# Kernel tuning notes

Hardware: AMD Instinct MI355X
Metric: run time of the kernel (lower is better)

## Reference

```python
import jax, jax.numpy as jnp
import numpy as np


def _conv(x, w, pad):
    # NCHW conv, stride 1
    return jax.lax.conv_general_dilated(
        x, w, window_strides=(1, 1), padding=pad,
        dimension_numbers=('NCHW', 'OIHW', 'NCHW'))


def setup_inputs() -> dict:
    key = jax.random.key(0)
    ks = jax.random.split(key, 8)
    N, Cin, H, W = 8, 512, 64, 64
    Cout, scale = 128, 2
    sd = 0.02
    return {
        'x':     jax.random.normal(ks[0], (N, Cin, H, W), jnp.float32),
        'w_du':  jax.random.normal(ks[1], (Cout, Cin, 3, 1), jnp.float32) * sd,
        'b_du':  jnp.zeros((Cout,), jnp.float32),
        'w_lr':  jax.random.normal(ks[2], (Cout, Cin, 1, 3), jnp.float32) * sd,
        'b_lr':  jnp.zeros((Cout,), jnp.float32),
        'w_1x1': jax.random.normal(ks[3], (Cout, Cin, 1, 1), jnp.float32) * sd,
        'w_ch':  jax.random.normal(ks[4], (Cout, 3 * Cout, 1, 1), jnp.float32) * sd,
        'w_w':   jax.random.normal(ks[5], (Cout * scale, Cout, 1, 1), jnp.float32) * sd,
        'w_H':   jax.random.normal(ks[6], (Cout * scale, Cout, 1, 1), jnp.float32) * sd,
        'scale': scale,
    }


def _conv_du(x, w, b):
    # convDU3, stride=1: the (3,1) conv is applied to each 1-tall row slice with
    # padding (1,0); rows are folded into the batch dim (vectorized, same math).
    N, C, H, W = x.shape
    rows = x.transpose(0, 2, 1, 3).reshape(N * H, C, 1, W)
    y = _conv(rows, w, ((1, 1), (0, 0))) + b[None, :, None, None]
    y = jax.nn.relu(y)                       # (N*H, Cout, 1, W)
    Co = y.shape[1]
    return y.reshape(N, H, Co, W).transpose(0, 2, 1, 3)


def _conv_lr(x, w, b):
    # convLR3, stride=1: (1,3) conv per 1-wide column slice; columns -> batch.
    N, C, H, W = x.shape
    cols = x.transpose(0, 3, 1, 2).reshape(N * W, C, H, 1)
    y = _conv(cols, w, ((0, 0), (1, 1))) + b[None, :, None, None]
    y = jax.nn.relu(y)                       # (N*W, Cout, H, 1)
    Co = y.shape[1]
    return y.reshape(N, W, Co, H).transpose(0, 2, 3, 1)


def reference(x, w_du, b_du, w_lr, b_lr, w_1x1, w_ch, w_w, w_H, scale):
    xdu = _conv_du(x, w_du, b_du)
    xlr = _conv_lr(x, w_lr, b_lr)
    x1 = _conv(x, w_1x1, ((0, 0), (0, 0)))
    x = jnp.concatenate((x1, xlr, xdu), axis=1)
    x = _conv(x, w_ch, ((0, 0), (0, 0)))
    x = _conv(x, w_w, ((0, 0), (0, 0)))      # (N, Cout*scale, H, W)
    N, C, H, W = x.shape
    # height pixel-shuffle: channels -> height
    xp = x.transpose(0, 3, 2, 1).reshape(N, W, H * scale, C // scale)
    xp = xp.transpose(0, 3, 2, 1)            # (N, Cout, H*scale, W)
    xh = _conv(xp, w_H, ((0, 0), (0, 0)))    # (N, Cout*scale, H*scale, W)
    # width pixel-shuffle: channels -> width
    xh = xh.transpose(0, 2, 3, 1).reshape(N, H * scale, W * scale, C // scale)
    return xh.transpose(0, 3, 1, 2)          # (N, Cout, H*scale, W*scale)
```

## Files before the change

### kernel.cpp

```cpp
#include <hip/hip_runtime.h>
#include <hip/hip_bf16.h>
#include <stdint.h>
#include <stddef.h>


typedef __attribute__((ext_vector_type(8))) __bf16 bf16x8;
typedef __attribute__((ext_vector_type(4))) float  f32x4;
typedef __attribute__((ext_vector_type(2))) float  f32x2;
typedef __attribute__((ext_vector_type(4))) unsigned int u32x4;
typedef __attribute__((ext_vector_type(2))) unsigned int u32x2;

#define BAR() asm volatile("s_waitcnt lgkmcnt(0)\n\ts_barrier" ::: "memory")



__global__ __launch_bounds__(256) void prep_k(
    const float* __restrict__ w_ch, const float* __restrict__ w_1x1,
    const float* __restrict__ w_lr, const float* __restrict__ w_du,
    const float* __restrict__ w_H,  const float* __restrict__ w_w,
    __bf16* __restrict__ Wf, __bf16* __restrict__ W2f)
{
  __shared__ float wh[2][128];
  __shared__ float Mrow[2][128];
  int bid = blockIdx.x;
  if (bid < 768) {
    int gid = bid * 256 + threadIdx.x;
    int r = gid >> 9, c = gid & 511;
    float v;
    if (r < 128) {
      const float* a_ = w_ch + r * 384;
      const float* b_ = w_1x1 + c;
      float s0 = 0.f, s1 = 0.f, s2 = 0.f, s3 = 0.f;
      #pragma unroll
      for (int j = 0; j < 128; j += 4) {
        s0 += a_[j + 0] * b_[(size_t)(j + 0) * 512];
        s1 += a_[j + 1] * b_[(size_t)(j + 1) * 512];
        s2 += a_[j + 2] * b_[(size_t)(j + 2) * 512];
        s3 += a_[j + 3] * b_[(size_t)(j + 3) * 512];
      }
      v = (s0 + s1) + (s2 + s3);
    } else if (r < 256) {
      v = w_lr[(r - 128) * 1536 + c * 3 + 1];
    } else {
      v = w_du[(r - 256) * 1536 + c * 3 + 1];
    }
    int gks = c >> 5, lsub = (c >> 3) & 3, jj = c & 7;
    int mfrag = r >> 4, lrow = r & 15;
    Wf[((gks * 24 + mfrag) << 9) + ((lrow + 16 * lsub) << 3) + jj] = (__bf16)v;
  } else {
    int t = threadIdx.x & 127, half = threadIdx.x >> 7;
    int r = (bid - 768) * 2 + half;
    int beta = r >> 8, gam = r & 1, irow = (r >> 1) & 127;
    wh[half][t] = w_H[(gam * 128 + irow) * 128 + t];
    __syncthreads();
    {
      const float* ww = w_w + beta * 16384 + t;
      float s0 = 0.f, s1 = 0.f, s2 = 0.f, s3 = 0.f;
      #pragma unroll
      for (int s = 0; s < 128; s += 4) {
        s0 += wh[half][s + 0] * ww[(s + 0) * 128];
        s1 += wh[half][s + 1] * ww[(s + 1) * 128];
        s2 += wh[half][s + 2] * ww[(s + 2) * 128];
        s3 += wh[half][s + 3] * ww[(s + 3) * 128];
      }
      Mrow[half][t] = (s0 + s1) + (s2 + s3);
    }
    __syncthreads();
    int mfrag = r >> 4, lrow = r & 15;
    #pragma unroll
    for (int c0 = 0; c0 < 384; c0 += 128) {
      int col = c0 + t;
      float v;
      if (c0 == 0) {
        v = Mrow[half][t];
      } else {
        const float* wc = w_ch + col;
        float s0 = 0.f, s1 = 0.f, s2 = 0.f, s3 = 0.f;
        #pragma unroll
        for (int k = 0; k < 128; k += 4) {
          s0 += Mrow[half][k + 0] * wc[(k + 0) * 384];
          s1 += Mrow[half][k + 1] * wc[(k + 1) * 384];
          s2 += Mrow[half][k + 2] * wc[(k + 2) * 384];
          s3 += Mrow[half][k + 3] * wc[(k + 3) * 384];
        }
        v = (s0 + s1) + (s2 + s3);
      }
      int gks = col >> 5, lsub = (col >> 3) & 3, jj = col & 7;
      W2f[((gks * 32 + mfrag) << 9) + ((lrow + 16 * lsub) << 3) + jj] = (__bf16)v;
    }
  }
}


__device__ __forceinline__ int swzB(int px) {
  return (((px & 7) ^ ((px >> 3) & 7)) << 4);
}

__global__ __launch_bounds__(512, 4) void fused_k(
    const float* __restrict__ x, const __bf16* __restrict__ Wf,
    const __bf16* __restrict__ W2f,
    const float* __restrict__ b_lr, const float* __restrict__ b_du,
    float* __restrict__ out)
{
  __shared__ __align__(16) char smem[49152 + 16384];
  char* Tlds = smem;
  char* buf0 = smem + 49152;
  char* buf1 = smem + 49152 + 8192;

  const int tid  = threadIdx.x;
  const int lane = tid & 63;
  const int wv   = tid >> 6;
  const int l15  = lane & 15, lg = lane >> 4;

  const int p0      = blockIdx.x * 64;
  const int img     = p0 >> 12;
  const int pixbase = p0 & 4095;
  const float* xb   = x + (size_t)img * (512 * 4096) + pixbase;
  const char* Wfb   = (const char*)Wf;
  const char* W2b   = (const char*)W2f;

  const int sp4 = (tid & 15) * 4;
  const int skp = (tid >> 4) * 2;

  f32x4 ldv[2];
  auto issueS = [&](int kt) {
    ldv[0] = *(const f32x4*)(xb + (size_t)(kt * 64 + skp) * 4096 + sp4);
    ldv[1] = *(const f32x4*)(xb + (size_t)(kt * 64 + skp + 1) * 4096 + sp4);
  };
  auto writeS = [&](char* bw) {
    #pragma unroll
    for (int pi = 0; pi < 4; ++pi) {
      int px = sp4 + pi;
      union { __bf16 b[2]; unsigned int u; } wd;
      wd.b[0] = (__bf16)ldv[0][pi];
      wd.b[1] = (__bf16)ldv[1][pi];
      *(unsigned int*)(bw + px * 128 + ((skp * 2) ^ swzB(px))) = wd.u;
    }
  };

  f32x4 acc1[3][4] = {};

  auto compute1 = [&](int kt, const char* bbuf) {
    #pragma unroll
    for (int ks = 0; ks < 2; ++ks) {
      bf16x8 af[3];
      #pragma unroll
      for (int i = 0; i < 3; ++i)
        af[i] = *(const bf16x8*)(Wfb +
            (((kt * 2 + ks) * 24 + wv * 3 + i) << 10) + lane * 16);
      bf16x8 bfr[4];
      #pragma unroll
      for (int j = 0; j < 4; ++j) {
        int rb = j * 16 + l15;
        bfr[j] = *(const bf16x8*)(bbuf + rb * 128 +
                                  ((ks * 64 + lg * 16) ^ swzB(rb)));
      }
      __builtin_amdgcn_s_setprio(1);
      #pragma unroll
      for (int i = 0; i < 3; ++i)
        #pragma unroll
        for (int j = 0; j < 4; ++j)
          acc1[i][j] = __builtin_amdgcn_mfma_f32_16x16x32_bf16(
              af[i], bfr[j], acc1[i][j], 0, 0, 0);
      __builtin_amdgcn_s_setprio(0);
    }
  };

  issueS(0);
  writeS(buf0);
  issueS(1);
  BAR();

  #pragma unroll 1
  for (int kt = 0; kt < 8; ++kt) {
    const char* bcur = (kt & 1) ? buf1 : buf0;
    char* bnext      = (kt & 1) ? buf0 : buf1;
    compute1(kt, bcur);
    if (kt < 7) {
      writeS(bnext);
      if (kt < 6) issueS(kt + 2);
      BAR();
    }
  }

  #pragma unroll
  for (int i = 0; i < 3; ++i) {
    int m0 = wv * 48 + i * 16 + lg * 4;
    bool rl = (m0 >= 128);
    const float* bp = (m0 >= 256) ? (b_du + (m0 - 256)) : (b_lr + (m0 - 128));
    float b0 = 0.f, b1 = 0.f, b2 = 0.f, b3 = 0.f;
    if (rl) { b0 = bp[0]; b1 = bp[1]; b2 = bp[2]; b3 = bp[3]; }
    #pragma unroll
    for (int j = 0; j < 4; ++j) {
      int p = j * 16 + l15;
      union { __bf16 b[4]; u32x2 u; } wd;
      float v0 = acc1[i][j][0], v1 = acc1[i][j][1];
      float v2 = acc1[i][j][2], v3 = acc1[i][j][3];
      if (rl) {
        v0 = fmaxf(v0 + b0, 0.f); v1 = fmaxf(v1 + b1, 0.f);
        v2 = fmaxf(v2 + b2, 0.f); v3 = fmaxf(v3 + b3, 0.f);
      }
      wd.b[0] = (__bf16)v0; wd.b[1] = (__bf16)v1;
      wd.b[2] = (__bf16)v2; wd.b[3] = (__bf16)v3;
      *(u32x2*)(Tlds + p * 768 + ((m0 * 2) ^ ((p & 7) << 4))) = wd.u;
    }
  }
  BAR();

  f32x4 acc2[4][4] = {};
  bf16x8 afA[4], afB[4];
  #pragma unroll
  for (int i = 0; i < 4; ++i)
    afA[i] = *(const bf16x8*)(W2b + ((0 * 32 + wv * 4 + i) << 10) + lane * 16);

  #pragma unroll 1
  for (int g2 = 0; g2 < 6; ++g2) {
    int gA = 2 * g2, gB = 2 * g2 + 1;
    #pragma unroll
    for (int i = 0; i < 4; ++i)
      afB[i] = *(const bf16x8*)(W2b + ((gB * 32 + wv * 4 + i) << 10) + lane * 16);
    {
      bf16x8 bfr[4];
      #pragma unroll
      for (int j = 0; j < 4; ++j) {
        int rb = j * 16 + l15;
        bfr[j] = *(const bf16x8*)(Tlds + rb * 768 +
                                  ((gA * 64 + lg * 16) ^ ((rb & 7) << 4)));
      }
      __builtin_amdgcn_s_setprio(1);
      #pragma unroll
      for (int i = 0; i < 4; ++i)
        #pragma unroll
        for (int j = 0; j < 4; ++j)
          acc2[i][j] = __builtin_amdgcn_mfma_f32_16x16x32_bf16(
              afA[i], bfr[j], acc2[i][j], 0, 0, 0);
      __builtin_amdgcn_s_setprio(0);
    }
    if (g2 < 5) {
      #pragma unroll
      for (int i = 0; i < 4; ++i)
        afA[i] = *(const bf16x8*)(W2b + (((gA + 2) * 32 + wv * 4 + i) << 10) + lane * 16);
    }
    {
      bf16x8 bfr[4];
      #pragma unroll
      for (int j = 0; j < 4; ++j) {
        int rb = j * 16 + l15;
        bfr[j] = *(const bf16x8*)(Tlds + rb * 768 +
                                  ((gB * 64 + lg * 16) ^ ((rb & 7) << 4)));
      }
      __builtin_amdgcn_s_setprio(1);
      #pragma unroll
      for (int i = 0; i < 4; ++i)
        #pragma unroll
        for (int j = 0; j < 4; ++j)
          acc2[i][j] = __builtin_amdgcn_mfma_f32_16x16x32_bf16(
              afB[i], bfr[j], acc2[i][j], 0, 0, 0);
      __builtin_amdgcn_s_setprio(0);
    }
  }

  #pragma unroll
  for (int i = 0; i < 4; ++i) {
    int r = (wv * 4 + i) * 16 + lg * 4;
    int beta = r >> 8;
    int irow = (r >> 1) & 127;
    #pragma unroll
    for (int j = 0; j < 4; ++j) {
      int pp = pixbase + j * 16 + l15;
      int h = pp >> 6, w = pp & 63;
      size_t o0 = ((((size_t)img * 128 + irow) * 128) + (2 * h + beta)) * 128
                  + 2 * w;
      f32x2 lo; lo.x = acc2[i][j][0]; lo.y = acc2[i][j][1];
      f32x2 hi; hi.x = acc2[i][j][2]; hi.y = acc2[i][j][3];
      *(f32x2*)(out + o0)         = lo;
      *(f32x2*)(out + o0 + 16384) = hi;
    }
  }
}


extern "C" void kernel_launch(void* const* d_in, const int* in_sizes, int n_in,
                              void* d_out, int out_size, void* d_ws, size_t ws_size,
                              hipStream_t stream) {
  const float* x     = (const float*)d_in[0];
  const float* w_du  = (const float*)d_in[1];
  const float* b_du  = (const float*)d_in[2];
  const float* w_lr  = (const float*)d_in[3];
  const float* b_lr  = (const float*)d_in[4];
  const float* w_1x1 = (const float*)d_in[5];
  const float* w_ch  = (const float*)d_in[6];
  const float* w_w   = (const float*)d_in[7];
  const float* w_H   = (const float*)d_in[8];
  float* out = (float*)d_out;

  char* ws = (char*)d_ws;
  __bf16* Wf  = (__bf16*)(ws + 0);
  __bf16* W2f = (__bf16*)(ws + 393216);
  if (ws_size < (size_t)786432) return;

  prep_k <<<1024, 256, 0, stream>>>(w_ch, w_1x1, w_lr, w_du, w_H, w_w, Wf, W2f);
  fused_k<<<512, 512, 0, stream>>>(x, Wf, W2f, b_lr, b_du, out);
}
```

Measured before the change: 48.26 us.

## Process two pixel tiles per block, overlapping stage-2 GEMM with next tile's stage-1

Each block now handles 128 pixels as two 64-pixel tiles with double-buffered intermediate LDS. The second GEMM for tile A is interleaved with the first GEMM for tile B, so MFMA work can hide the global loads of x and the barriers. The grid is halved to 256 blocks and LDS grows to 112KB, so occupancy drops to at most two blocks per CU and fewer blocks are left to fill the 256 CUs.

```diff
diff --git a/kernel.cpp b/kernel.cpp
--- a/kernel.cpp
+++ b/kernel.cpp
@@ -96,34 +96,37 @@
   return (((px & 7) ^ ((px >> 3) & 7)) << 4);
 }
 
-__global__ __launch_bounds__(512, 4) void fused_k(
+__global__ __launch_bounds__(512, 2) void fused_k(
     const float* __restrict__ x, const __bf16* __restrict__ Wf,
     const __bf16* __restrict__ W2f,
     const float* __restrict__ b_lr, const float* __restrict__ b_du,
     float* __restrict__ out)
 {
-  __shared__ __align__(16) char smem[49152 + 16384];
-  char* Tlds = smem;
-  char* buf0 = smem + 49152;
-  char* buf1 = smem + 49152 + 8192;
+  __shared__ __align__(16) char smem[114688];
+  char* Tlds0 = smem;
+  char* Tlds1 = smem + 49152;
+  char* buf0  = smem + 98304;
+  char* buf1  = smem + 98304 + 8192;
 
   const int tid  = threadIdx.x;
   const int lane = tid & 63;
   const int wv   = tid >> 6;
   const int l15  = lane & 15, lg = lane >> 4;
 
-  const int p0      = blockIdx.x * 64;
-  const int img     = p0 >> 12;
-  const int pixbase = p0 & 4095;
-  const float* xb   = x + (size_t)img * (512 * 4096) + pixbase;
-  const char* Wfb   = (const char*)Wf;
-  const char* W2b   = (const char*)W2f;
+  const int p0   = blockIdx.x * 128;
+  const int img  = p0 >> 12;
+  const int pixA = p0 & 4095;
+  const int pixB = pixA + 64;
+  const float* xbA = x + (size_t)img * (512 * 4096) + pixA;
+  const float* xbB = xbA + 64;
+  const char* Wfb  = (const char*)Wf;
+  const char* W2b  = (const char*)W2f;
 
   const int sp4 = (tid & 15) * 4;
   const int skp = (tid >> 4) * 2;
 
   f32x4 ldv[2];
-  auto issueS = [&](int kt) {
+  auto issueS = [&](const float* xb, int kt) {
     ldv[0] = *(const f32x4*)(xb + (size_t)(kt * 64 + skp) * 4096 + sp4);
     ldv[1] = *(const f32x4*)(xb + (size_t)(kt * 64 + skp + 1) * 4096 + sp4);
   };
@@ -138,7 +141,16 @@
     }
   };
 
-  f32x4 acc1[3][4] = {};
+  f32x4 acc1[3][4];
+  f32x4 acc2[4][4];
+  #pragma unroll
+  for (int i = 0; i < 3; ++i)
+    #pragma unroll
+    for (int j = 0; j < 4; ++j) acc1[i][j] = f32x4{0.f, 0.f, 0.f, 0.f};
+  #pragma unroll
+  for (int i = 0; i < 4; ++i)
+    #pragma unroll
+    for (int j = 0; j < 4; ++j) acc2[i][j] = f32x4{0.f, 0.f, 0.f, 0.f};
 
   auto compute1 = [&](int kt, const char* bbuf) {
     #pragma unroll
@@ -166,117 +178,147 @@
     }
   };
 
-  issueS(0);
+  auto epi1 = [&](char* Tl) {
+    #pragma unroll
+    for (int i = 0; i < 3; ++i) {
+      int m0 = wv * 48 + i * 16 + lg * 4;
+      bool rl = (m0 >= 128);
+      const float* bp = (m0 >= 256) ? (b_du + (m0 - 256)) : (b_lr + (m0 - 128));
+      float b0 = 0.f, b1 = 0.f, b2 = 0.f, b3 = 0.f;
+      if (rl) { b0 = bp[0]; b1 = bp[1]; b2 = bp[2]; b3 = bp[3]; }
+      #pragma unroll
+      for (int j = 0; j < 4; ++j) {
+        int p = j * 16 + l15;
+        union { __bf16 b[4]; u32x2 u; } wd;
+        float v0 = acc1[i][j][0], v1 = acc1[i][j][1];
+        float v2 = acc1[i][j][2], v3 = acc1[i][j][3];
+        if (rl) {
+          v0 = fmaxf(v0 + b0, 0.f); v1 = fmaxf(v1 + b1, 0.f);
+          v2 = fmaxf(v2 + b2, 0.f); v3 = fmaxf(v3 + b3, 0.f);
+        }
+        wd.b[0] = (__bf16)v0; wd.b[1] = (__bf16)v1;
+        wd.b[2] = (__bf16)v2; wd.b[3] = (__bf16)v3;
+        *(u32x2*)(Tl + p * 768 + ((m0 * 2) ^ ((p & 7) << 4))) = wd.u;
+      }
+    }
+  };
+
+  bf16x8 af2A[4], af2B[4];
+  auto loadAf2 = [&](int g, bf16x8* af) {
+    #pragma unroll
+    for (int i = 0; i < 4; ++i)
+      af[i] = *(const bf16x8*)(W2b + ((g * 32 + wv * 4 + i) << 10) + lane * 16);
+  };
+  auto P2step = [&](int g, const bf16x8* af, const char* Tl) {
+    bf16x8 bfr[4];
+    #pragma unroll
+    for (int j = 0; j < 4; ++j) {
+      int rb = j * 16 + l15;
+      bfr[j] = *(const bf16x8*)(Tl + rb * 768 +
+                                ((g * 64 + lg * 16) ^ ((rb & 7) << 4)));
+    }
+    __builtin_amdgcn_s_setprio(1);
+    #pragma unroll
+    for (int i = 0; i < 4; ++i)
+      #pragma unroll
+      for (int j = 0; j < 4; ++j)
+        acc2[i][j] = __builtin_amdgcn_mfma_f32_16x16x32_bf16(
+            af[i], bfr[j], acc2[i][j], 0, 0, 0);
+    __builtin_amdgcn_s_setprio(0);
+  };
+
+  auto storeOut = [&](int pixb) {
+    #pragma unroll
+    for (int i = 0; i < 4; ++i) {
+      int r = wv * 64 + i * 16 + lg * 4;
+      int beta = r >> 8;
+      int irow = (r >> 1) & 127;
+      #pragma unroll
+      for (int j = 0; j < 4; ++j) {
+        int pp = pixb + j * 16 + l15;
+        int h = pp >> 6, w = pp & 63;
+        size_t o0 = ((((size_t)img * 128 + irow) * 128) + (2 * h + beta)) * 128
+                    + 2 * w;
+        f32x2 lo; lo.x = acc2[i][j][0]; lo.y = acc2[i][j][1];
+        f32x2 hi; hi.x = acc2[i][j][2]; hi.y = acc2[i][j][3];
+        *(f32x2*)(out + o0)         = lo;
+        *(f32x2*)(out + o0 + 16384) = hi;
+      }
+    }
+  };
+
+  issueS(xbA, 0);
   writeS(buf0);
-  issueS(1);
+  issueS(xbA, 1);
   BAR();
-
   #pragma unroll 1
-  for (int kt = 0; kt < 8; ++kt) {
-    const char* bcur = (kt & 1) ? buf1 : buf0;
-    char* bnext      = (kt & 1) ? buf0 : buf1;
-    compute1(kt, bcur);
-    if (kt < 7) {
-      writeS(bnext);
-      if (kt < 6) issueS(kt + 2);
+  for (int kt2 = 0; kt2 < 8; kt2 += 2) {
+    compute1(kt2, buf0);
+    writeS(buf1);
+    if (kt2 < 6) issueS(xbA, kt2 + 2);
+    BAR();
+    compute1(kt2 + 1, buf1);
+    if (kt2 < 6) {
+      writeS(buf0);
+      issueS(xbA, kt2 + 3);
       BAR();
     }
   }
 
+  issueS(xbB, 0);
+  epi1(Tlds0);
+  writeS(buf0);
+  issueS(xbB, 1);
   #pragma unroll
-  for (int i = 0; i < 3; ++i) {
-    int m0 = wv * 48 + i * 16 + lg * 4;
-    bool rl = (m0 >= 128);
-    const float* bp = (m0 >= 256) ? (b_du + (m0 - 256)) : (b_lr + (m0 - 128));
-    float b0 = 0.f, b1 = 0.f, b2 = 0.f, b3 = 0.f;
-    if (rl) { b0 = bp[0]; b1 = bp[1]; b2 = bp[2]; b3 = bp[3]; }
-    #pragma unroll
-    for (int j = 0; j < 4; ++j) {
-      int p = j * 16 + l15;
-      union { __bf16 b[4]; u32x2 u; } wd;
-      float v0 = acc1[i][j][0], v1 = acc1[i][j][1];
-      float v2 = acc1[i][j][2], v3 = acc1[i][j][3];
-      if (rl) {
-        v0 = fmaxf(v0 + b0, 0.f); v1 = fmaxf(v1 + b1, 0.f);
-        v2 = fmaxf(v2 + b2, 0.f); v3 = fmaxf(v3 + b3, 0.f);
-      }
-      wd.b[0] = (__bf16)v0; wd.b[1] = (__bf16)v1;
-      wd.b[2] = (__bf16)v2; wd.b[3] = (__bf16)v3;
-      *(u32x2*)(Tlds + p * 768 + ((m0 * 2) ^ ((p & 7) << 4))) = wd.u;
-    }
-  }
+  for (int i = 0; i < 3; ++i)
+    #pragma unroll
+    for (int j = 0; j < 4; ++j) acc1[i][j] = f32x4{0.f, 0.f, 0.f, 0.f};
+  loadAf2(0, af2A);
   BAR();
 
-  f32x4 acc2[4][4] = {};
-  bf16x8 afA[4], afB[4];
+  #pragma unroll 1
+  for (int g2 = 0; g2 < 8; g2 += 2) {
+    loadAf2(g2 + 1, af2B);
+    P2step(g2, af2A, Tlds0);
+    compute1(g2, buf0);
+    writeS(buf1);
+    if (g2 < 6) issueS(xbB, g2 + 2);
+    BAR();
+    loadAf2(g2 + 2, af2A);
+    P2step(g2 + 1, af2B, Tlds0);
+    compute1(g2 + 1, buf1);
+    if (g2 < 6) {
+      writeS(buf0);
+      issueS(xbB, g2 + 3);
+      BAR();
+    }
+  }
+
+  #pragma unroll 1
+  for (int g2 = 8; g2 < 12; g2 += 2) {
+    loadAf2(g2 + 1, af2B);
+    P2step(g2, af2A, Tlds0);
+    if (g2 < 10) loadAf2(g2 + 2, af2A);
+    P2step(g2 + 1, af2B, Tlds0);
+  }
+
+  storeOut(pixA);
+  epi1(Tlds1);
   #pragma unroll
   for (int i = 0; i < 4; ++i)
-    afA[i] = *(const bf16x8*)(W2b + ((0 * 32 + wv * 4 + i) << 10) + lane * 16);
+    #pragma unroll
+    for (int j = 0; j < 4; ++j) acc2[i][j] = f32x4{0.f, 0.f, 0.f, 0.f};
+  loadAf2(0, af2A);
+  BAR();
 
   #pragma unroll 1
-  for (int g2 = 0; g2 < 6; ++g2) {
-    int gA = 2 * g2, gB = 2 * g2 + 1;
-    #pragma unroll
-    for (int i = 0; i < 4; ++i)
-      afB[i] = *(const bf16x8*)(W2b + ((gB * 32 + wv * 4 + i) << 10) + lane * 16);
-    {
-      bf16x8 bfr[4];
-      #pragma unroll
-      for (int j = 0; j < 4; ++j) {
-        int rb = j * 16 + l15;
-        bfr[j] = *(const bf16x8*)(Tlds + rb * 768 +
-                                  ((gA * 64 + lg * 16) ^ ((rb & 7) << 4)));
-      }
-      __builtin_amdgcn_s_setprio(1);
-      #pragma unroll
-      for (int i = 0; i < 4; ++i)
-        #pragma unroll
-        for (int j = 0; j < 4; ++j)
-          acc2[i][j] = __builtin_amdgcn_mfma_f32_16x16x32_bf16(
-              afA[i], bfr[j], acc2[i][j], 0, 0, 0);
-      __builtin_amdgcn_s_setprio(0);
-    }
-    if (g2 < 5) {
-      #pragma unroll
-      for (int i = 0; i < 4; ++i)
-        afA[i] = *(const bf16x8*)(W2b + (((gA + 2) * 32 + wv * 4 + i) << 10) + lane * 16);
-    }
-    {
-      bf16x8 bfr[4];
-      #pragma unroll
-      for (int j = 0; j < 4; ++j) {
-        int rb = j * 16 + l15;
-        bfr[j] = *(const bf16x8*)(Tlds + rb * 768 +
-                                  ((gB * 64 + lg * 16) ^ ((rb & 7) << 4)));
-      }
-      __builtin_amdgcn_s_setprio(1);
-      #pragma unroll
-      for (int i = 0; i < 4; ++i)
-        #pragma unroll
-        for (int j = 0; j < 4; ++j)
-          acc2[i][j] = __builtin_amdgcn_mfma_f32_16x16x32_bf16(
-              afB[i], bfr[j], acc2[i][j], 0, 0, 0);
-      __builtin_amdgcn_s_setprio(0);
-    }
-  }
-
-  #pragma unroll
-  for (int i = 0; i < 4; ++i) {
-    int r = (wv * 4 + i) * 16 + lg * 4;
-    int beta = r >> 8;
-    int irow = (r >> 1) & 127;
-    #pragma unroll
-    for (int j = 0; j < 4; ++j) {
-      int pp = pixbase + j * 16 + l15;
-      int h = pp >> 6, w = pp & 63;
-      size_t o0 = ((((size_t)img * 128 + irow) * 128) + (2 * h + beta)) * 128
-                  + 2 * w;
-      f32x2 lo; lo.x = acc2[i][j][0]; lo.y = acc2[i][j][1];
-      f32x2 hi; hi.x = acc2[i][j][2]; hi.y = acc2[i][j][3];
-      *(f32x2*)(out + o0)         = lo;
-      *(f32x2*)(out + o0 + 16384) = hi;
-    }
-  }
+  for (int g2 = 0; g2 < 12; g2 += 2) {
+    loadAf2(g2 + 1, af2B);
+    P2step(g2, af2A, Tlds1);
+    if (g2 < 10) loadAf2(g2 + 2, af2A);
+    P2step(g2 + 1, af2B, Tlds1);
+  }
+  storeOut(pixB);
 }
 
 
@@ -300,5 +342,5 @@
   if (ws_size < (size_t)786432) return;
 
   prep_k <<<1024, 256, 0, stream>>>(w_ch, w_1x1, w_lr, w_du, w_H, w_w, Wf, W2f);
-  fused_k<<<512, 512, 0, stream>>>(x, Wf, W2f, b_lr, b_du, out);
+  fused_k<<<256, 512, 0, stream>>>(x, Wf, W2f, b_lr, b_du, out);
 }
```

Measured after the change: 54.59 us. 1.13x slower.
